# Performance work log

Hardware: AMD Instinct MI355X
Metric: run time of the kernel (lower is better)

The kernel has to match this reference:

```python
import jax, jax.numpy as jnp
import numpy as np

LAMBDA_REG = 0.1


def setup_inputs() -> dict:
    key = jax.random.key(0)
    k1, k2, k3, k4 = jax.random.split(key, 4)
    B, C, D = 4096, 10000, 128
    logits = jax.random.normal(k1, (B, C), dtype=jnp.float32)
    margins = jax.random.uniform(k2, (C,), dtype=jnp.float32)
    weights = jax.random.normal(k3, (C, D), dtype=jnp.float32)
    label = jax.random.randint(k4, (B,), 0, C, dtype=jnp.int64)
    return {"logits": logits, "margins": margins, "weights": weights, "label": label}


def reference(logits, margins, weights, label):
    B, C = logits.shape
    rows = jnp.arange(B)

    # F.cross_entropy(logits, label): mean NLL of log_softmax
    logp = jax.nn.log_softmax(logits, axis=-1)
    ce = -jnp.mean(logp[rows, label])

    # margin regularization
    margin_reg = LAMBDA_REG * jnp.mean(margins)

    # intra-class angular loss
    theta_yi = jnp.arccos(jnp.clip(logits[rows, label] / LAMBDA_REG, -1.0, 1.0))
    intra_loss = jnp.mean(theta_yi) / jnp.pi

    # inter-class loss: sum_i sum_{j != y_i} acos(clamp(w_{y_i} . w_j))
    # Vectorized replacement of the O(B*C) Python double loop:
    wy = weights[label]                       # (B, D) gather of ground-truth class rows
    S = jnp.einsum('bd,cd->bc', wy, weights)  # (B, C) pairwise dot products
    A = jnp.arccos(jnp.clip(S, -1.0, 1.0))    # (B, C) angles
    inter_sum = jnp.sum(A) - jnp.sum(A[rows, label])  # exclude j == y_i terms
    inter_loss = inter_sum / (B * (C - 1) * jnp.pi)

    return ce + margin_reg + intra_loss + inter_loss
```

## Files before the change

kernel.cpp:

```cpp
#include <hip/hip_runtime.h>
#include <stdint.h>
#include <math.h>

typedef __attribute__((ext_vector_type(8))) __bf16 bf16x8;
typedef __attribute__((ext_vector_type(4))) float floatx4;

constexpr int kB = 4096;
constexpr int kC = 10000;
constexpr int kD = 128;
constexpr int kNT = 79;
constexpr int kMT = 32;
constexpr int kBricksB = kNT * 32;
constexpr int kBricksA = kMT * 32;
constexpr int kPrepBlocks = (kBricksB + kBricksA) / 4;
constexpr float kPI = 3.14159265358979323846f;
constexpr float kLambda = 0.1f;
constexpr float kInvInter = (float)(1.0 / (4096.0 * 9999.0 * 3.141592653589793));

constexpr int kCEBlocks = kB / 4;
constexpr int kInterBlocks = kNT * kMT;

constexpr size_t kBrickBytes = (size_t)(kBricksB + kBricksA) * 1024;
constexpr int kPartMargin = 0;
constexpr int kPartCE = 1;
constexpr int kPartInter = 1 + kB;
constexpr int kNumPart = 1 + kB + kNT * kMT;

__device__ __forceinline__ float fast_acos(float x) {
    float t = fabsf(x);
    float s = sqrtf(fmaxf(1.0f - t, 0.0f));
    float p = fmaf(fmaf(fmaf(-0.0187293f, t, 0.0742610f), t, -0.2121144f),
                   t, 1.5707288f);
    float r = s * p;
    return x < 0.0f ? kPI - r : r;
}

__device__ __forceinline__ uint16_t f2bf(float f) {
    union { float f; uint32_t u; } c; c.f = f;
    uint32_t u = c.u;
    uint32_t r = (u + 0x7FFFu + ((u >> 16) & 1u)) >> 16;
    return (uint16_t)r;
}

__global__ __launch_bounds__(256) void prep_kernel(
    const float* __restrict__ W, const float* __restrict__ margins,
    const int* __restrict__ label, uint16_t* __restrict__ wsB,
    uint16_t* __restrict__ wsA, float* __restrict__ part) {
    int blk = blockIdx.x;
    if (blk < kPrepBlocks) {
        int brick = blk * 4 + (threadIdx.x >> 6);
        int lane = threadIdx.x & 63;
        bool isA = brick >= kBricksB;
        int b2 = isA ? (brick - kBricksB) : brick;
        int kk = b2 & 3;
        int rb = (b2 >> 2) & 7;
        int tile = b2 >> 5;
        int row = tile * 128 + rb * 16 + (lane & 15);
        int k = kk * 32 + (lane >> 4) * 8;
        float v[8];
        if (isA) {
            int r = label[row];
            const float* src = W + (size_t)r * kD + k;
            #pragma unroll
            for (int j = 0; j < 8; ++j) v[j] = src[j];
        } else if (row < kC) {
            const float* src = W + (size_t)row * kD + k;
            #pragma unroll
            for (int j = 0; j < 8; ++j) v[j] = src[j];
        } else {
            #pragma unroll
            for (int j = 0; j < 8; ++j) v[j] = 0.0f;
        }
        uint4 pk;
        pk.x = (uint32_t)f2bf(v[0]) | ((uint32_t)f2bf(v[1]) << 16);
        pk.y = (uint32_t)f2bf(v[2]) | ((uint32_t)f2bf(v[3]) << 16);
        pk.z = (uint32_t)f2bf(v[4]) | ((uint32_t)f2bf(v[5]) << 16);
        pk.w = (uint32_t)f2bf(v[6]) | ((uint32_t)f2bf(v[7]) << 16);
        uint4* dst = (uint4*)(isA ? wsA : wsB);
        dst[(size_t)b2 * 64 + lane] = pk;
    } else {
        float s = 0.0f;
        for (int i = threadIdx.x; i < kC; i += 256) s += margins[i];
        for (int off = 32; off; off >>= 1) s += __shfl_down(s, off);
        __shared__ float p[4];
        if ((threadIdx.x & 63) == 0) p[threadIdx.x >> 6] = s;
        __syncthreads();
        if (threadIdx.x == 0)
            part[kPartMargin] = (p[0] + p[1] + p[2] + p[3]) * (kLambda / (float)kC);
    }
}

__global__ __launch_bounds__(256) void inter_kernel(
    const uint16_t* __restrict__ wsA, const uint16_t* __restrict__ wsB,
    float* __restrict__ part) {
    __shared__ float red[4];
    int ii = blockIdx.x;
    int mt = ii / kNT;
    int nt = ii - mt * kNT;
    int tid = threadIdx.x;
    int wave = tid >> 6, lane = tid & 63;
    int wr = wave >> 1, wc = wave & 1;

    const char* gA = (const char*)wsA + (size_t)mt * 32768;
    const char* gB = (const char*)wsB + (size_t)nt * 32768;

    floatx4 zero = {0.0f, 0.0f, 0.0f, 0.0f};
    floatx4 acc[4][4];
    #pragma unroll
    for (int i = 0; i < 4; ++i)
        #pragma unroll
        for (int jj = 0; jj < 4; ++jj) acc[i][jj] = zero;

    #pragma unroll
    for (int kk = 0; kk < 4; ++kk) {
        bf16x8 a[4], bfr[4];
        #pragma unroll
        for (int i = 0; i < 4; ++i) {
            a[i] = *(const bf16x8*)(gA + ((wr * 4 + i) * 4 + kk) * 1024 +
                                    lane * 16);
            bfr[i] = *(const bf16x8*)(gB + ((wc * 4 + i) * 4 + kk) * 1024 +
                                      lane * 16);
        }
        #pragma unroll
        for (int i = 0; i < 4; ++i)
            #pragma unroll
            for (int jj = 0; jj < 4; ++jj)
                acc[i][jj] = __builtin_amdgcn_mfma_f32_16x16x32_bf16(
                    a[i], bfr[jj], acc[i][jj], 0, 0, 0);
    }

    float local = 0.0f;
    int col0 = nt * 128 + wc * 64 + (lane & 15);
    #pragma unroll
    for (int jj = 0; jj < 4; ++jj) {
        if (col0 + jj * 16 < kC) {
            #pragma unroll
            for (int i = 0; i < 4; ++i)
                #pragma unroll
                for (int r = 0; r < 4; ++r)
                    local += fast_acos(fminf(fmaxf(acc[i][jj][r], -1.0f), 1.0f));
        }
    }
    for (int off = 32; off; off >>= 1) local += __shfl_down(local, off);
    if (lane == 0) red[wave] = local;
    __syncthreads();
    if (tid == 0)
        part[kPartInter + ii] = (red[0] + red[1] + red[2] + red[3]) * kInvInter;
}

__global__ __launch_bounds__(256) void ce_kernel(
    const float* __restrict__ logits, const int* __restrict__ label,
    float* __restrict__ part) {
    int tid = threadIdx.x;
    int wave = tid >> 6, lane = tid & 63;
    int row = blockIdx.x * 4 + wave;
    const float* lp = logits + (size_t)row * kC;
    const floatx4* lp4 = (const floatx4*)lp;
    int lbl = label[row];
    float z = lp[lbl];
    float s0 = 0.0f, s1 = 0.0f, s2 = 0.0f, s3 = 0.0f;
    floatx4 v[13], w[13];
    bool hastail = lane < kC / 4 - 39 * 64;
    floatx4 vt;

    #pragma unroll
    for (int k = 0; k < 13; ++k)
        v[k] = __builtin_nontemporal_load(&lp4[lane + k * 64]);
    #pragma unroll
    for (int k = 0; k < 13; ++k)
        w[k] = __builtin_nontemporal_load(&lp4[lane + (13 + k) * 64]);
    #pragma unroll
    for (int k = 0; k < 13; ++k) {
        s0 += __expf(v[k].x); s1 += __expf(v[k].y);
        s2 += __expf(v[k].z); s3 += __expf(v[k].w);
    }
    #pragma unroll
    for (int k = 0; k < 13; ++k)
        v[k] = __builtin_nontemporal_load(&lp4[lane + (26 + k) * 64]);
    #pragma unroll
    for (int k = 0; k < 13; ++k) {
        s0 += __expf(w[k].x); s1 += __expf(w[k].y);
        s2 += __expf(w[k].z); s3 += __expf(w[k].w);
    }
    if (hastail) vt = __builtin_nontemporal_load(&lp4[39 * 64 + lane]);
    #pragma unroll
    for (int k = 0; k < 13; ++k) {
        s0 += __expf(v[k].x); s1 += __expf(v[k].y);
        s2 += __expf(v[k].z); s3 += __expf(v[k].w);
    }
    if (hastail) {
        s0 += __expf(vt.x); s1 += __expf(vt.y);
        s2 += __expf(vt.z); s3 += __expf(vt.w);
    }
    float s = (s0 + s1) + (s2 + s3);
    for (int off = 32; off; off >>= 1) s += __shfl_down(s, off);
    if (lane == 0) {
        float ce = __logf(s) - z;
        float intra = fast_acos(fminf(fmaxf(z * (1.0f / kLambda), -1.0f), 1.0f));
        part[kPartCE + row] = ce * (1.0f / kB) + intra * (1.0f / (kB * kPI));
    }
}

__global__ __launch_bounds__(256) void finalize_kernel(
    const float* __restrict__ part, float* __restrict__ out, int out_size) {
    float s = 0.0f;
    for (int i = threadIdx.x; i < kNumPart; i += 256) s += part[i];
    for (int off = 32; off; off >>= 1) s += __shfl_down(s, off);
    __shared__ float p[4];
    if ((threadIdx.x & 63) == 0) p[threadIdx.x >> 6] = s;
    __syncthreads();
    if (threadIdx.x == 0) out[0] = p[0] + p[1] + p[2] + p[3];
    for (int i = 1 + threadIdx.x; i < out_size; i += 256) out[i] = 0.0f;
}

extern "C" void kernel_launch(void* const* d_in, const int* in_sizes, int n_in,
                              void* d_out, int out_size, void* d_ws, size_t ws_size,
                              hipStream_t stream) {
    const float* logits = (const float*)d_in[0];
    const float* margins = (const float*)d_in[1];
    const float* W = (const float*)d_in[2];
    const int* label = (const int*)d_in[3];
    float* out = (float*)d_out;

    uint16_t* wsB = (uint16_t*)d_ws;
    uint16_t* wsA = (uint16_t*)((char*)d_ws + (size_t)kNT * 32768);
    float* part = (float*)((char*)d_ws + kBrickBytes);

    prep_kernel<<<kPrepBlocks + 1, 256, 0, stream>>>(W, margins, label, wsB, wsA, part);
    inter_kernel<<<kInterBlocks, 256, 0, stream>>>(wsA, wsB, part);
    ce_kernel<<<kCEBlocks, 256, 0, stream>>>(logits, label, part);
    finalize_kernel<<<1, 256, 0, stream>>>(part, out, out_size);
}
```

Before: 279.5 us.

## Fuse CE into prep kernel and stage inter GEMM tiles through LDS

Merges the cross-entropy row kernel into the weight-prep launch as extra blocks, removing one kernel launch and letting the bandwidth-bound logits pass overlap with the bf16 weight packing. The inter-class GEMM kernel now copies its 64 KB A and B tiles into shared memory with coalesced loads before the MFMA loop, instead of issuing fragment loads straight from global memory. This costs 64 KB of LDS per block, which limits occupancy, and adds a barrier before compute.

```diff
diff --git a/kernel.cpp b/kernel.cpp
--- a/kernel.cpp
+++ b/kernel.cpp
@@ -19,6 +19,7 @@
 
 constexpr int kCEBlocks = kB / 4;
 constexpr int kInterBlocks = kNT * kMT;
+constexpr int kL1Blocks = kCEBlocks + kPrepBlocks + 1;
 
 constexpr size_t kBrickBytes = (size_t)(kBricksB + kBricksA) * 1024;
 constexpr int kPartMargin = 0;
@@ -42,14 +43,66 @@
     return (uint16_t)r;
 }
 
-__global__ __launch_bounds__(256) void prep_kernel(
-    const float* __restrict__ W, const float* __restrict__ margins,
-    const int* __restrict__ label, uint16_t* __restrict__ wsB,
-    uint16_t* __restrict__ wsA, float* __restrict__ part) {
-    int blk = blockIdx.x;
-    if (blk < kPrepBlocks) {
-        int brick = blk * 4 + (threadIdx.x >> 6);
-        int lane = threadIdx.x & 63;
+__global__ __launch_bounds__(256) void prep_ce_kernel(
+    const float* __restrict__ logits, const float* __restrict__ W,
+    const float* __restrict__ margins, const int* __restrict__ label,
+    uint16_t* __restrict__ wsB, uint16_t* __restrict__ wsA,
+    float* __restrict__ part) {
+    int b = blockIdx.x;
+    int tid = threadIdx.x;
+    int wave = tid >> 6, lane = tid & 63;
+
+    if (b < kCEBlocks) {
+        int row = b * 4 + wave;
+        const float* lp = logits + (size_t)row * kC;
+        const floatx4* lp4 = (const floatx4*)lp;
+        int lbl = label[row];
+        float z = lp[lbl];
+        float s0 = 0.0f, s1 = 0.0f, s2 = 0.0f, s3 = 0.0f;
+        floatx4 v[13], w[13];
+        bool hastail = lane < kC / 4 - 39 * 64;
+        floatx4 vt;
+
+        #pragma unroll
+        for (int k = 0; k < 13; ++k)
+            v[k] = __builtin_nontemporal_load(&lp4[lane + k * 64]);
+        #pragma unroll
+        for (int k = 0; k < 13; ++k)
+            w[k] = __builtin_nontemporal_load(&lp4[lane + (13 + k) * 64]);
+        #pragma unroll
+        for (int k = 0; k < 13; ++k) {
+            s0 += __expf(v[k].x); s1 += __expf(v[k].y);
+            s2 += __expf(v[k].z); s3 += __expf(v[k].w);
+        }
+        #pragma unroll
+        for (int k = 0; k < 13; ++k)
+            v[k] = __builtin_nontemporal_load(&lp4[lane + (26 + k) * 64]);
+        #pragma unroll
+        for (int k = 0; k < 13; ++k) {
+            s0 += __expf(w[k].x); s1 += __expf(w[k].y);
+            s2 += __expf(w[k].z); s3 += __expf(w[k].w);
+        }
+        if (hastail) vt = __builtin_nontemporal_load(&lp4[39 * 64 + lane]);
+        #pragma unroll
+        for (int k = 0; k < 13; ++k) {
+            s0 += __expf(v[k].x); s1 += __expf(v[k].y);
+            s2 += __expf(v[k].z); s3 += __expf(v[k].w);
+        }
+        if (hastail) {
+            s0 += __expf(vt.x); s1 += __expf(vt.y);
+            s2 += __expf(vt.z); s3 += __expf(vt.w);
+        }
+        float s = (s0 + s1) + (s2 + s3);
+        for (int off = 32; off; off >>= 1) s += __shfl_down(s, off);
+        if (lane == 0) {
+            float ce = __logf(s) - z;
+            float intra =
+                fast_acos(fminf(fmaxf(z * (1.0f / kLambda), -1.0f), 1.0f));
+            part[kPartCE + row] = ce * (1.0f / kB) + intra * (1.0f / (kB * kPI));
+        }
+    } else if (b < kCEBlocks + kPrepBlocks) {
+        int blk = b - kCEBlocks;
+        int brick = blk * 4 + wave;
         bool isA = brick >= kBricksB;
         int b2 = isA ? (brick - kBricksB) : brick;
         int kk = b2 & 3;
@@ -80,12 +133,12 @@
         dst[(size_t)b2 * 64 + lane] = pk;
     } else {
         float s = 0.0f;
-        for (int i = threadIdx.x; i < kC; i += 256) s += margins[i];
+        for (int i = tid; i < kC; i += 256) s += margins[i];
         for (int off = 32; off; off >>= 1) s += __shfl_down(s, off);
         __shared__ float p[4];
-        if ((threadIdx.x & 63) == 0) p[threadIdx.x >> 6] = s;
+        if ((tid & 63) == 0) p[tid >> 6] = s;
         __syncthreads();
-        if (threadIdx.x == 0)
+        if (tid == 0)
             part[kPartMargin] = (p[0] + p[1] + p[2] + p[3]) * (kLambda / (float)kC);
     }
 }
@@ -93,6 +146,7 @@
 __global__ __launch_bounds__(256) void inter_kernel(
     const uint16_t* __restrict__ wsA, const uint16_t* __restrict__ wsB,
     float* __restrict__ part) {
+    __shared__ uint4 lds4[4096];
     __shared__ float red[4];
     int ii = blockIdx.x;
     int mt = ii / kNT;
@@ -101,8 +155,18 @@
     int wave = tid >> 6, lane = tid & 63;
     int wr = wave >> 1, wc = wave & 1;
 
-    const char* gA = (const char*)wsA + (size_t)mt * 32768;
-    const char* gB = (const char*)wsB + (size_t)nt * 32768;
+    const uint4* gA4 = (const uint4*)((const char*)wsA + (size_t)mt * 32768);
+    const uint4* gB4 = (const uint4*)((const char*)wsB + (size_t)nt * 32768);
+
+    #pragma unroll
+    for (int it = 0; it < 8; ++it) lds4[it * 256 + tid] = gA4[it * 256 + tid];
+    #pragma unroll
+    for (int it = 0; it < 8; ++it)
+        lds4[2048 + it * 256 + tid] = gB4[it * 256 + tid];
+    __syncthreads();
+
+    const char* lA = (const char*)lds4;
+    const char* lB = (const char*)lds4 + 32768;
 
     floatx4 zero = {0.0f, 0.0f, 0.0f, 0.0f};
     floatx4 acc[4][4];
@@ -116,9 +180,9 @@
         bf16x8 a[4], bfr[4];
         #pragma unroll
         for (int i = 0; i < 4; ++i) {
-            a[i] = *(const bf16x8*)(gA + ((wr * 4 + i) * 4 + kk) * 1024 +
+            a[i] = *(const bf16x8*)(lA + ((wr * 4 + i) * 4 + kk) * 1024 +
                                     lane * 16);
-            bfr[i] = *(const bf16x8*)(gB + ((wc * 4 + i) * 4 + kk) * 1024 +
+            bfr[i] = *(const bf16x8*)(lB + ((wc * 4 + i) * 4 + kk) * 1024 +
                                       lane * 16);
         }
         #pragma unroll
@@ -146,59 +210,6 @@
     __syncthreads();
     if (tid == 0)
         part[kPartInter + ii] = (red[0] + red[1] + red[2] + red[3]) * kInvInter;
-}
-
-__global__ __launch_bounds__(256) void ce_kernel(
-    const float* __restrict__ logits, const int* __restrict__ label,
-    float* __restrict__ part) {
-    int tid = threadIdx.x;
-    int wave = tid >> 6, lane = tid & 63;
-    int row = blockIdx.x * 4 + wave;
-    const float* lp = logits + (size_t)row * kC;
-    const floatx4* lp4 = (const floatx4*)lp;
-    int lbl = label[row];
-    float z = lp[lbl];
-    float s0 = 0.0f, s1 = 0.0f, s2 = 0.0f, s3 = 0.0f;
-    floatx4 v[13], w[13];
-    bool hastail = lane < kC / 4 - 39 * 64;
-    floatx4 vt;
-
-    #pragma unroll
-    for (int k = 0; k < 13; ++k)
-        v[k] = __builtin_nontemporal_load(&lp4[lane + k * 64]);
-    #pragma unroll
-    for (int k = 0; k < 13; ++k)
-        w[k] = __builtin_nontemporal_load(&lp4[lane + (13 + k) * 64]);
-    #pragma unroll
-    for (int k = 0; k < 13; ++k) {
-        s0 += __expf(v[k].x); s1 += __expf(v[k].y);
-        s2 += __expf(v[k].z); s3 += __expf(v[k].w);
-    }
-    #pragma unroll
-    for (int k = 0; k < 13; ++k)
-        v[k] = __builtin_nontemporal_load(&lp4[lane + (26 + k) * 64]);
-    #pragma unroll
-    for (int k = 0; k < 13; ++k) {
-        s0 += __expf(w[k].x); s1 += __expf(w[k].y);
-        s2 += __expf(w[k].z); s3 += __expf(w[k].w);
-    }
-    if (hastail) vt = __builtin_nontemporal_load(&lp4[39 * 64 + lane]);
-    #pragma unroll
-    for (int k = 0; k < 13; ++k) {
-        s0 += __expf(v[k].x); s1 += __expf(v[k].y);
-        s2 += __expf(v[k].z); s3 += __expf(v[k].w);
-    }
-    if (hastail) {
-        s0 += __expf(vt.x); s1 += __expf(vt.y);
-        s2 += __expf(vt.z); s3 += __expf(vt.w);
-    }
-    float s = (s0 + s1) + (s2 + s3);
-    for (int off = 32; off; off >>= 1) s += __shfl_down(s, off);
-    if (lane == 0) {
-        float ce = __logf(s) - z;
-        float intra = fast_acos(fminf(fmaxf(z * (1.0f / kLambda), -1.0f), 1.0f));
-        part[kPartCE + row] = ce * (1.0f / kB) + intra * (1.0f / (kB * kPI));
-    }
 }
 
 __global__ __launch_bounds__(256) void finalize_kernel(
@@ -226,8 +237,8 @@
     uint16_t* wsA = (uint16_t*)((char*)d_ws + (size_t)kNT * 32768);
     float* part = (float*)((char*)d_ws + kBrickBytes);
 
-    prep_kernel<<<kPrepBlocks + 1, 256, 0, stream>>>(W, margins, label, wsB, wsA, part);
+    prep_ce_kernel<<<kL1Blocks, 256, 0, stream>>>(logits, W, margins, label,
+                                                  wsB, wsA, part);
     inter_kernel<<<kInterBlocks, 256, 0, stream>>>(wsA, wsB, part);
-    ce_kernel<<<kCEBlocks, 256, 0, stream>>>(logits, label, part);
     finalize_kernel<<<1, 256, 0, stream>>>(part, out, out_size);
 }
```

Measured after the change: 281.8 us. No clear change (+0.8%).
